# Kernel tuning notes

Hardware: AMD Instinct MI355X
Metric: run time of the kernel (lower is better)

## Reference

```python
import jax, jax.numpy as jnp
import numpy as np

B, HG, WG, D, NH, K = 4, 32, 32, 768, 12, 7
HD = D // NH  # 64


def _neigh_idx(H, W, k):
    # NATTEN semantics: 7x7 window centered at the query, shifted (clamped)
    # at borders so every query has exactly k*k neighbors.
    si = np.clip(np.arange(H) - k // 2, 0, H - k)  # [H] window row starts
    sj = np.clip(np.arange(W) - k // 2, 0, W - k)  # [W] window col starts
    ri = si[:, None] + np.arange(k)[None, :]       # [H, k]
    cj = sj[:, None] + np.arange(k)[None, :]       # [W, k]
    idx = ri[:, None, :, None] * W + cj[None, :, None, :]  # [H, W, k, k]
    return jnp.asarray(idx.reshape(H * W, k * k), dtype=jnp.int32)


def setup_inputs() -> dict:
    key = jax.random.key(0)
    ks = jax.random.split(key, 3)
    s = D ** -0.5
    return {
        "x": jax.random.normal(ks[0], (B, HG * WG, D), dtype=jnp.float32),
        "qkv_w": jax.random.normal(ks[1], (3 * D, D), dtype=jnp.float32) * s,
        "qkv_b": jnp.zeros((3 * D,), dtype=jnp.float32),
        "proj_w": jax.random.normal(ks[2], (D, D), dtype=jnp.float32) * s,
        "proj_b": jnp.zeros((D,), dtype=jnp.float32),
    }


def reference(x, qkv_w, qkv_b, proj_w, proj_b):
    b, n, d = x.shape  # n == HG*WG
    idx = _neigh_idx(HG, WG, K)  # [n, K*K] flat neighbor token indices

    qkv = x @ qkv_w.T + qkv_b                      # [b, n, 3d]
    q, k, v = jnp.split(qkv, 3, axis=-1)
    q = q.reshape(b, n, NH, HD) * (HD ** -0.5)     # [b, n, h, hd]
    k = k.reshape(b, n, NH, HD)
    v = v.reshape(b, n, NH, HD)

    kn = jnp.take(k, idx, axis=1)                  # [b, n, 49, h, hd]
    vn = jnp.take(v, idx, axis=1)                  # [b, n, 49, h, hd]

    scores = jnp.einsum('bnhd,bnkhd->bnhk', q, kn)  # [b, n, h, 49]
    attn = jax.nn.softmax(scores, axis=-1)
    out = jnp.einsum('bnhk,bnkhd->bnhd', attn, vn).reshape(b, n, d)
    return out @ proj_w.T + proj_b
```

## Files before the change

kernel.cpp:

```cpp
#include <hip/hip_runtime.h>


typedef __bf16 bf16x8 __attribute__((ext_vector_type(8)));
typedef short s16x4 __attribute__((ext_vector_type(4)));
typedef float f32x4 __attribute__((ext_vector_type(4)));

__device__ __forceinline__ unsigned short f2bf(float f) {
  unsigned u = __float_as_uint(f);
  u += 0x7fffu + ((u >> 16) & 1u);
  return (unsigned short)(u >> 16);
}

template <typename T>
__device__ __forceinline__ void gld_lds16(const T* g, T* l) {
  __builtin_amdgcn_global_load_lds((const __attribute__((address_space(1))) void*)g,
                                   (__attribute__((address_space(3))) void*)l, 16, 0, 0);
}

__global__ void cvt_kernel(const float* __restrict__ x, const float* __restrict__ w1,
                           const float* __restrict__ w2, unsigned short* __restrict__ xo,
                           unsigned short* __restrict__ w1o, unsigned short* __restrict__ w2o) {
  const int n1 = 4096 * 768 / 4;
  const int n2 = 2304 * 768 / 4;
  const int n3 = 768 * 768 / 4;
  int i = blockIdx.x * 256 + threadIdx.x;
  float4 v;
  unsigned short* dst;
  int o;
  if (i < n1) {
    o = i; v = ((const float4*)x)[o]; dst = xo;
  } else if (i < n1 + n2) {
    o = i - n1; v = ((const float4*)w1)[o]; dst = w1o;
  } else if (i < n1 + n2 + n3) {
    o = i - n1 - n2; v = ((const float4*)w2)[o]; dst = w2o;
  } else {
    return;
  }
  ushort4 r;
  r.x = f2bf(v.x); r.y = f2bf(v.y); r.z = f2bf(v.z); r.w = f2bf(v.w);
  ((ushort4*)dst)[o] = r;
}

template <int MODE>
__global__ __launch_bounds__(256) void gemm_bt(const unsigned short* __restrict__ A,
                                               const unsigned short* __restrict__ Bm,
                                               const float* __restrict__ bias,
                                               unsigned short* __restrict__ obf,
                                               unsigned short* __restrict__ vtout,
                                               float* __restrict__ of32,
                                               int M, int N, int Kd) {
  __shared__ __align__(16) unsigned short sA[2][128 * 32];
  __shared__ __align__(16) unsigned short sB[2][128 * 32];
  const int tid = threadIdx.x;
  const int lane = tid & 63;
  const int wv = tid >> 6;

  constexpr int HX = (MODE == 0) ? 9 : 3;
  constexpr int HY = 8;
  const int lin = blockIdx.y * gridDim.x + blockIdx.x;
  const int xcd = lin & 7, rrr = lin >> 3;
  const int bx = (xcd & 1) * HX + rrr % HX;
  const int by = (xcd >> 1) * HY + rrr / HX;
  const int m0 = by * 128, n0 = bx * 128;

  const int wrow = (wv >> 1) * 64, wcol = (wv & 1) * 64;
  const int lr = lane & 15, lq = lane >> 4;
  const int rchunk = (lq ^ ((lr >> 1) & 3)) * 8;

  f32x4 acc[4][4] = {};

  const int schunk = ((tid & 3) ^ ((tid >> 3) & 3)) * 8;
  const unsigned short* gA = A + (size_t)(m0 + (tid >> 2)) * Kd + schunk;
  const unsigned short* gB = Bm + (size_t)(n0 + (tid >> 2)) * Kd + schunk;

  gld_lds16(gA, &sA[0][tid * 8]);
  gld_lds16(gA + (size_t)64 * Kd, &sA[0][2048 + tid * 8]);
  gld_lds16(gB, &sB[0][tid * 8]);
  gld_lds16(gB + (size_t)64 * Kd, &sB[0][2048 + tid * 8]);
  __syncthreads();

  int cur = 0;
  for (int k0 = 0; k0 < Kd; k0 += 32) {
    const int nxt = k0 + 32;
    if (nxt < Kd) {
      unsigned short* dA = sA[cur ^ 1];
      unsigned short* dB = sB[cur ^ 1];
      gld_lds16(gA + nxt, dA + tid * 8);
      gld_lds16(gA + (size_t)64 * Kd + nxt, dA + 2048 + tid * 8);
      gld_lds16(gB + nxt, dB + tid * 8);
      gld_lds16(gB + (size_t)64 * Kd + nxt, dB + 2048 + tid * 8);
    }
    const unsigned short* cA = sA[cur];
    const unsigned short* cB = sB[cur];
    bf16x8 af[4], bfr[4];
#pragma unroll
    for (int t = 0; t < 4; ++t) {
      af[t] = *(const bf16x8*)(cA + (wrow + t * 16 + lr) * 32 + rchunk);
      bfr[t] = *(const bf16x8*)(cB + (wcol + t * 16 + lr) * 32 + rchunk);
    }
#pragma unroll
    for (int im = 0; im < 4; ++im)
#pragma unroll
      for (int in = 0; in < 4; ++in)
        acc[im][in] = __builtin_amdgcn_mfma_f32_16x16x32_bf16(af[im], bfr[in], acc[im][in], 0, 0, 0);
    __syncthreads();
    cur ^= 1;
  }

  if (MODE == 0) {
    const int sidx = n0 / 768;
    if (sidx == 2) {
#pragma unroll
      for (int im = 0; im < 4; ++im) {
#pragma unroll
        for (int in = 0; in < 4; ++in) {
          int gn = n0 + wcol + in * 16 + lr;
          int rem = gn - 1536;
          int hh = rem >> 6, dd = gn & 63;
          float bsv = bias[gn];
          int gm0 = m0 + wrow + im * 16 + lq * 4;
          ushort4 pk;
          pk.x = f2bf(acc[im][in][0] + bsv);
          pk.y = f2bf(acc[im][in][1] + bsv);
          pk.z = f2bf(acc[im][in][2] + bsv);
          pk.w = f2bf(acc[im][in][3] + bsv);
          *(ushort4*)(vtout + (size_t)(hh * 64 + dd) * 4096 + gm0) = pk;
        }
      }
    } else {
      const float scale = (sidx == 0) ? 0.18033688f : 1.0f;
#pragma unroll
      for (int im = 0; im < 4; ++im) {
#pragma unroll
        for (int in = 0; in < 4; ++in) {
          int gn = n0 + wcol + in * 16 + lr;
          int rem = gn - sidx * 768;
          int hh = rem >> 6, dd = gn & 63;
          float bsv = bias[gn];
#pragma unroll
          for (int r = 0; r < 4; ++r) {
            int gm = m0 + wrow + im * 16 + lq * 4 + r;
            float val = (acc[im][in][r] + bsv) * scale;
            obf[((size_t)(sidx * 12 + hh) * 4096 + gm) * 64 + dd] = f2bf(val);
          }
        }
      }
    }
  } else {
#pragma unroll
    for (int im = 0; im < 4; ++im) {
#pragma unroll
      for (int in = 0; in < 4; ++in) {
        int gn = n0 + wcol + in * 16 + lr;
        float bsv = bias[gn];
#pragma unroll
        for (int r = 0; r < 4; ++r) {
          int gm = m0 + wrow + im * 16 + lq * 4 + r;
          of32[(size_t)gm * N + gn] = acc[im][in][r] + bsv;
        }
      }
    }
  }
}

__global__ __launch_bounds__(256, 2) void natten_kernel(const unsigned short* __restrict__ qkvt,
                                                        unsigned short* __restrict__ aout) {
  __shared__ __align__(16) unsigned short sQ[64 * 64];
  __shared__ __align__(16) unsigned short sK[256 * 64];
  __shared__ __align__(16) unsigned short sVt[64 * 256];
  const int h = blockIdx.x, ip = blockIdx.y, b = blockIdx.z;
  const int i0 = ip * 2;
  const int tid = threadIdx.x, lane = tid & 63, wv = tid >> 6;
  const int lg = lane >> 4, lm = lane & 15;
  int si0 = i0 - 3; si0 = si0 < 0 ? 0 : si0; if (si0 > 25) si0 = 25;
  const int gb = b * 1024;
  const unsigned short* Qg = qkvt + ((size_t)h * 4096 + gb + i0 * 32) * 64;
  const unsigned short* Kg = qkvt + ((size_t)(12 + h) * 4096 + gb) * 64;
  const unsigned short* Vg = qkvt + (size_t)24 * 4096 * 64 + (size_t)h * 64 * 4096 + gb;

#pragma unroll
  for (int it = 0; it < 2; ++it) {
    int f = it * 256 + tid;
    int q = f >> 3, c16 = f & 7;
    uint4 v = *(const uint4*)(Qg + q * 64 + c16 * 8);
    int s = q & 15;
    *(uint2*)(sQ + q * 64 + ((((c16 << 1)) ^ s) << 2)) = make_uint2(v.x, v.y);
    *(uint2*)(sQ + q * 64 + ((((c16 << 1) | 1) ^ s) << 2)) = make_uint2(v.z, v.w);
  }
#pragma unroll
  for (int it = 0; it < 8; ++it) {
    int f = it * 256 + tid;
    int t = f >> 3, c16 = f & 7;
    int wr = t >> 5, c = t & 31;
    int row = si0 + wr; if (row > 31) row = 31;
    uint4 v = *(const uint4*)(Kg + (row * 32 + c) * 64 + c16 * 8);
    int s = t & 15;
    *(uint2*)(sK + t * 64 + ((((c16 << 1)) ^ s) << 2)) = make_uint2(v.x, v.y);
    *(uint2*)(sK + t * 64 + ((((c16 << 1) | 1) ^ s) << 2)) = make_uint2(v.z, v.w);
  }
#pragma unroll
  for (int it = 0; it < 8; ++it) {
    int f = it * 256 + tid;
    int d = f >> 5, tc16 = f & 31;
    int wr = tc16 >> 2;
    int row = si0 + wr; if (row > 31) row = 31;
    uint4 v = *(const uint4*)(Vg + (size_t)d * 4096 + row * 32 + (tc16 & 3) * 8);
    int s = d & 15;
    *(uint2*)(sVt + d * 256 + ((((tc16 << 1)) ^ s) << 2)) = make_uint2(v.x, v.y);
    *(uint2*)(sVt + d * 256 + ((((tc16 << 1) | 1) ^ s) << 2)) = make_uint2(v.z, v.w);
  }
  __syncthreads();

  const int row_sel = wv >> 1;
  const int jhalf = wv & 1;
  const int i = i0 + row_sel;
  int si_w = i - 3; si_w = si_w < 0 ? 0 : si_w; if (si_w > 25) si_w = 25;
  const int toff = (si_w - si0) * 32;
  const int j = jhalf * 16 + lm;
  int sj = j - 3; sj = sj < 0 ? 0 : sj; if (sj > 25) sj = 25;

  float madd[2][4];
#pragma unroll
  for (int p = 0; p < 2; ++p)
#pragma unroll
    for (int r = 0; r < 4; ++r) {
      int c = p * 16 + lg * 4 + r;
      madd[p][r] = (c >= sj && c <= sj + 6) ? 0.f : -1e30f;
    }

  s16x4 qf[4];
  const int qrow = row_sel * 32 + j;
#pragma unroll
  for (int ks = 0; ks < 4; ++ks)
    qf[ks] = *(const s16x4*)(sQ + qrow * 64 + ((((ks << 2) + lg) ^ (qrow & 15)) << 2));

  f32x4 accS[14];
#pragma unroll
  for (int tt = 0; tt < 14; ++tt) {
    f32x4 a = {0.f, 0.f, 0.f, 0.f};
    const int trow = toff + tt * 16 + lm;
    const unsigned short* kr = sK + trow * 64;
    const int sw = trow & 15;
#pragma unroll
    for (int ks = 0; ks < 4; ++ks) {
      s16x4 kf = *(const s16x4*)(kr + ((((ks << 2) + lg) ^ sw) << 2));
      a = __builtin_amdgcn_mfma_f32_16x16x16bf16_1k(kf, qf[ks], a, 0, 0, 0);
    }
    accS[tt] = a;
  }

  float mx = -3e38f;
#pragma unroll
  for (int tt = 0; tt < 14; ++tt)
#pragma unroll
    for (int r = 0; r < 4; ++r) {
      float v = accS[tt][r] + madd[tt & 1][r];
      accS[tt][r] = v;
      mx = fmaxf(mx, v);
    }
  mx = fmaxf(mx, __shfl_xor(mx, 16, 64));
  mx = fmaxf(mx, __shfl_xor(mx, 32, 64));
  float sum = 0.f;
#pragma unroll
  for (int tt = 0; tt < 14; ++tt)
#pragma unroll
    for (int r = 0; r < 4; ++r) {
      float p = exp2f(accS[tt][r] - mx);
      accS[tt][r] = p;
      sum += p;
    }
  sum += __shfl_xor(sum, 16, 64);
  sum += __shfl_xor(sum, 32, 64);
  const float inv = 1.f / sum;

  s16x4 pf[14];
#pragma unroll
  for (int tt = 0; tt < 14; ++tt) {
    union { unsigned u[2]; s16x4 v; } pk;
    pk.u[0] = ((unsigned)f2bf(accS[tt][1]) << 16) | f2bf(accS[tt][0]);
    pk.u[1] = ((unsigned)f2bf(accS[tt][3]) << 16) | f2bf(accS[tt][2]);
    pf[tt] = pk.v;
  }

  f32x4 accO[4] = {};
  const int choff = toff >> 2;
#pragma unroll
  for (int tt = 0; tt < 14; ++tt) {
    const int c8 = choff + tt * 4 + lg;
#pragma unroll
    for (int nt = 0; nt < 4; ++nt) {
      const int d = nt * 16 + lm;
      s16x4 vf = *(const s16x4*)(sVt + d * 256 + ((c8 ^ (d & 15)) << 2));
      accO[nt] = __builtin_amdgcn_mfma_f32_16x16x16bf16_1k(pf[tt], vf, accO[nt], 0, 0, 0);
    }
  }

  float invr[4];
#pragma unroll
  for (int r = 0; r < 4; ++r) invr[r] = __shfl(inv, lg * 4 + r, 64);

  const int tokbase = gb + i * 32 + jhalf * 16;
#pragma unroll
  for (int nt = 0; nt < 4; ++nt)
#pragma unroll
    for (int r = 0; r < 4; ++r) {
      int tok = tokbase + lg * 4 + r;
      aout[(size_t)tok * 768 + h * 64 + nt * 16 + lm] = f2bf(accO[nt][r] * invr[r]);
    }
}

extern "C" void kernel_launch(void* const* d_in, const int* in_sizes, int n_in,
                              void* d_out, int out_size, void* d_ws, size_t ws_size,
                              hipStream_t stream) {
  const float* x      = (const float*)d_in[0];
  const float* qkv_w  = (const float*)d_in[1];
  const float* qkv_b  = (const float*)d_in[2];
  const float* proj_w = (const float*)d_in[3];
  const float* proj_b = (const float*)d_in[4];
  char* ws = (char*)d_ws;

  unsigned short* xb    = (unsigned short*)(ws);
  unsigned short* wqkv  = (unsigned short*)(ws + 6291456);
  unsigned short* wproj = (unsigned short*)(ws + 9830400);
  unsigned short* qkvt  = (unsigned short*)(ws + 11010048);
  unsigned short* attnb = (unsigned short*)(ws + 29884416);
  unsigned short* vt    = qkvt + (size_t)24 * 4096 * 64;
  float* out = (float*)d_out;

  cvt_kernel<<<5376, 256, 0, stream>>>(x, qkv_w, proj_w, xb, wqkv, wproj);
  gemm_bt<0><<<dim3(18, 32), 256, 0, stream>>>(xb, wqkv, qkv_b, qkvt, vt, nullptr, 4096, 2304, 768);
  natten_kernel<<<dim3(12, 16, 4), 256, 0, stream>>>(qkvt, attnb);
  gemm_bt<1><<<dim3(6, 32), 256, 0, stream>>>(attnb, wproj, proj_b, nullptr, nullptr, out, 4096, 768, 768);
}
```

Measured before the change: 145.2 us.

## Share one LDS buffer for K and V in natten, retile projection GEMM

The natten kernel drops the separate Q, K and Vt shared buffers. It loads K and V into registers up front, reads Q straight from global memory, and reuses a single LDS buffer for K and then V with extra barriers between the phases. The smaller LDS footprint allows the launch bound to rise to 3 blocks per CU for higher occupancy and more latency hiding. The output projection GEMM is templated and moved to 64x64 tiles with a larger grid for better CU fill, at the cost of less data reuse per tile and more register pressure in natten.

```diff
diff --git a/kernel.cpp b/kernel.cpp
--- a/kernel.cpp
+++ b/kernel.cpp
@@ -41,7 +41,7 @@
   ((ushort4*)dst)[o] = r;
 }
 
-template <int MODE>
+template <int MODE, int BM, int BN>
 __global__ __launch_bounds__(256) void gemm_bt(const unsigned short* __restrict__ A,
                                                const unsigned short* __restrict__ Bm,
                                                const float* __restrict__ bias,
@@ -49,34 +49,36 @@
                                                unsigned short* __restrict__ vtout,
                                                float* __restrict__ of32,
                                                int M, int N, int Kd) {
-  __shared__ __align__(16) unsigned short sA[2][128 * 32];
-  __shared__ __align__(16) unsigned short sB[2][128 * 32];
+  constexpr int RA = BM / 64, RB = BN / 64;
+  constexpr int MI = BM / 32, NI = BN / 32;
+  __shared__ __align__(16) unsigned short sA[2][BM * 32];
+  __shared__ __align__(16) unsigned short sB[2][BN * 32];
   const int tid = threadIdx.x;
   const int lane = tid & 63;
   const int wv = tid >> 6;
 
-  constexpr int HX = (MODE == 0) ? 9 : 3;
-  constexpr int HY = 8;
+  constexpr int HX = (MODE == 0) ? 9 : 6;
+  constexpr int HY = (MODE == 0) ? 8 : 16;
   const int lin = blockIdx.y * gridDim.x + blockIdx.x;
   const int xcd = lin & 7, rrr = lin >> 3;
   const int bx = (xcd & 1) * HX + rrr % HX;
   const int by = (xcd >> 1) * HY + rrr / HX;
-  const int m0 = by * 128, n0 = bx * 128;
-
-  const int wrow = (wv >> 1) * 64, wcol = (wv & 1) * 64;
+  const int m0 = by * BM, n0 = bx * BN;
+
+  const int wrow = (wv >> 1) * (BM / 2), wcol = (wv & 1) * (BN / 2);
   const int lr = lane & 15, lq = lane >> 4;
   const int rchunk = (lq ^ ((lr >> 1) & 3)) * 8;
 
-  f32x4 acc[4][4] = {};
+  f32x4 acc[MI][NI] = {};
 
   const int schunk = ((tid & 3) ^ ((tid >> 3) & 3)) * 8;
   const unsigned short* gA = A + (size_t)(m0 + (tid >> 2)) * Kd + schunk;
   const unsigned short* gB = Bm + (size_t)(n0 + (tid >> 2)) * Kd + schunk;
 
-  gld_lds16(gA, &sA[0][tid * 8]);
-  gld_lds16(gA + (size_t)64 * Kd, &sA[0][2048 + tid * 8]);
-  gld_lds16(gB, &sB[0][tid * 8]);
-  gld_lds16(gB + (size_t)64 * Kd, &sB[0][2048 + tid * 8]);
+#pragma unroll
+  for (int r = 0; r < RA; ++r) gld_lds16(gA + (size_t)(r * 64) * Kd, &sA[0][r * 2048 + tid * 8]);
+#pragma unroll
+  for (int r = 0; r < RB; ++r) gld_lds16(gB + (size_t)(r * 64) * Kd, &sB[0][r * 2048 + tid * 8]);
   __syncthreads();
 
   int cur = 0;
@@ -85,23 +87,22 @@
     if (nxt < Kd) {
       unsigned short* dA = sA[cur ^ 1];
       unsigned short* dB = sB[cur ^ 1];
-      gld_lds16(gA + nxt, dA + tid * 8);
-      gld_lds16(gA + (size_t)64 * Kd + nxt, dA + 2048 + tid * 8);
-      gld_lds16(gB + nxt, dB + tid * 8);
-      gld_lds16(gB + (size_t)64 * Kd + nxt, dB + 2048 + tid * 8);
+#pragma unroll
+      for (int r = 0; r < RA; ++r) gld_lds16(gA + (size_t)(r * 64) * Kd + nxt, dA + r * 2048 + tid * 8);
+#pragma unroll
+      for (int r = 0; r < RB; ++r) gld_lds16(gB + (size_t)(r * 64) * Kd + nxt, dB + r * 2048 + tid * 8);
     }
     const unsigned short* cA = sA[cur];
     const unsigned short* cB = sB[cur];
-    bf16x8 af[4], bfr[4];
-#pragma unroll
-    for (int t = 0; t < 4; ++t) {
-      af[t] = *(const bf16x8*)(cA + (wrow + t * 16 + lr) * 32 + rchunk);
-      bfr[t] = *(const bf16x8*)(cB + (wcol + t * 16 + lr) * 32 + rchunk);
-    }
-#pragma unroll
-    for (int im = 0; im < 4; ++im)
-#pragma unroll
-      for (int in = 0; in < 4; ++in)
+    bf16x8 af[MI], bfr[NI];
+#pragma unroll
+    for (int t = 0; t < MI; ++t) af[t] = *(const bf16x8*)(cA + (wrow + t * 16 + lr) * 32 + rchunk);
+#pragma unroll
+    for (int t = 0; t < NI; ++t) bfr[t] = *(const bf16x8*)(cB + (wcol + t * 16 + lr) * 32 + rchunk);
+#pragma unroll
+    for (int im = 0; im < MI; ++im)
+#pragma unroll
+      for (int in = 0; in < NI; ++in)
         acc[im][in] = __builtin_amdgcn_mfma_f32_16x16x32_bf16(af[im], bfr[in], acc[im][in], 0, 0, 0);
     __syncthreads();
     cur ^= 1;
@@ -111,9 +112,9 @@
     const int sidx = n0 / 768;
     if (sidx == 2) {
 #pragma unroll
-      for (int im = 0; im < 4; ++im) {
-#pragma unroll
-        for (int in = 0; in < 4; ++in) {
+      for (int im = 0; im < MI; ++im) {
+#pragma unroll
+        for (int in = 0; in < NI; ++in) {
           int gn = n0 + wcol + in * 16 + lr;
           int rem = gn - 1536;
           int hh = rem >> 6, dd = gn & 63;
@@ -130,9 +131,9 @@
     } else {
       const float scale = (sidx == 0) ? 0.18033688f : 1.0f;
 #pragma unroll
-      for (int im = 0; im < 4; ++im) {
-#pragma unroll
-        for (int in = 0; in < 4; ++in) {
+      for (int im = 0; im < MI; ++im) {
+#pragma unroll
+        for (int in = 0; in < NI; ++in) {
           int gn = n0 + wcol + in * 16 + lr;
           int rem = gn - sidx * 768;
           int hh = rem >> 6, dd = gn & 63;
@@ -148,9 +149,9 @@
     }
   } else {
 #pragma unroll
-    for (int im = 0; im < 4; ++im) {
-#pragma unroll
-      for (int in = 0; in < 4; ++in) {
+    for (int im = 0; im < MI; ++im) {
+#pragma unroll
+      for (int in = 0; in < NI; ++in) {
         int gn = n0 + wcol + in * 16 + lr;
         float bsv = bias[gn];
 #pragma unroll
@@ -163,11 +164,9 @@
   }
 }
 
-__global__ __launch_bounds__(256, 2) void natten_kernel(const unsigned short* __restrict__ qkvt,
+__global__ __launch_bounds__(256, 3) void natten_kernel(const unsigned short* __restrict__ qkvt,
                                                         unsigned short* __restrict__ aout) {
-  __shared__ __align__(16) unsigned short sQ[64 * 64];
-  __shared__ __align__(16) unsigned short sK[256 * 64];
-  __shared__ __align__(16) unsigned short sVt[64 * 256];
+  __shared__ __align__(16) unsigned short sKV[256 * 64];
   const int h = blockIdx.x, ip = blockIdx.y, b = blockIdx.z;
   const int i0 = ip * 2;
   const int tid = threadIdx.x, lane = tid & 63, wv = tid >> 6;
@@ -178,38 +177,20 @@
   const unsigned short* Kg = qkvt + ((size_t)(12 + h) * 4096 + gb) * 64;
   const unsigned short* Vg = qkvt + (size_t)24 * 4096 * 64 + (size_t)h * 64 * 4096 + gb;
 
-#pragma unroll
-  for (int it = 0; it < 2; ++it) {
-    int f = it * 256 + tid;
-    int q = f >> 3, c16 = f & 7;
-    uint4 v = *(const uint4*)(Qg + q * 64 + c16 * 8);
-    int s = q & 15;
-    *(uint2*)(sQ + q * 64 + ((((c16 << 1)) ^ s) << 2)) = make_uint2(v.x, v.y);
-    *(uint2*)(sQ + q * 64 + ((((c16 << 1) | 1) ^ s) << 2)) = make_uint2(v.z, v.w);
-  }
+  uint4 kreg[8];
 #pragma unroll
   for (int it = 0; it < 8; ++it) {
-    int f = it * 256 + tid;
-    int t = f >> 3, c16 = f & 7;
-    int wr = t >> 5, c = t & 31;
+    int row = si0 + it; if (row > 31) row = 31;
+    kreg[it] = *(const uint4*)(Kg + (row * 32 + (tid >> 3)) * 64 + (tid & 7) * 8);
+  }
+  uint4 vreg[8];
+#pragma unroll
+  for (int it = 0; it < 8; ++it) {
+    int d = it * 8 + (tid >> 5);
+    int wr = (tid >> 2) & 7;
     int row = si0 + wr; if (row > 31) row = 31;
-    uint4 v = *(const uint4*)(Kg + (row * 32 + c) * 64 + c16 * 8);
-    int s = t & 15;
-    *(uint2*)(sK + t * 64 + ((((c16 << 1)) ^ s) << 2)) = make_uint2(v.x, v.y);
-    *(uint2*)(sK + t * 64 + ((((c16 << 1) | 1) ^ s) << 2)) = make_uint2(v.z, v.w);
-  }
-#pragma unroll
-  for (int it = 0; it < 8; ++it) {
-    int f = it * 256 + tid;
-    int d = f >> 5, tc16 = f & 31;
-    int wr = tc16 >> 2;
-    int row = si0 + wr; if (row > 31) row = 31;
-    uint4 v = *(const uint4*)(Vg + (size_t)d * 4096 + row * 32 + (tc16 & 3) * 8);
-    int s = d & 15;
-    *(uint2*)(sVt + d * 256 + ((((tc16 << 1)) ^ s) << 2)) = make_uint2(v.x, v.y);
-    *(uint2*)(sVt + d * 256 + ((((tc16 << 1) | 1) ^ s) << 2)) = make_uint2(v.z, v.w);
-  }
-  __syncthreads();
+    vreg[it] = *(const uint4*)(Vg + (size_t)d * 4096 + row * 32 + (tid & 3) * 8);
+  }
 
   const int row_sel = wv >> 1;
   const int jhalf = wv & 1;
@@ -219,6 +200,22 @@
   const int j = jhalf * 16 + lm;
   int sj = j - 3; sj = sj < 0 ? 0 : sj; if (sj > 25) sj = 25;
 
+  s16x4 qf[4];
+  const int qrow = row_sel * 32 + j;
+#pragma unroll
+  for (int ks = 0; ks < 4; ++ks)
+    qf[ks] = *(const s16x4*)(Qg + qrow * 64 + ks * 16 + lg * 4);
+
+#pragma unroll
+  for (int it = 0; it < 8; ++it) {
+    int t = it * 32 + (tid >> 3);
+    int c16 = tid & 7;
+    int s = t & 15;
+    *(uint2*)(sKV + t * 64 + ((((c16 << 1)) ^ s) << 2)) = make_uint2(kreg[it].x, kreg[it].y);
+    *(uint2*)(sKV + t * 64 + ((((c16 << 1) | 1) ^ s) << 2)) = make_uint2(kreg[it].z, kreg[it].w);
+  }
+  __syncthreads();
+
   float madd[2][4];
 #pragma unroll
   for (int p = 0; p < 2; ++p)
@@ -228,18 +225,12 @@
       madd[p][r] = (c >= sj && c <= sj + 6) ? 0.f : -1e30f;
     }
 
-  s16x4 qf[4];
-  const int qrow = row_sel * 32 + j;
-#pragma unroll
-  for (int ks = 0; ks < 4; ++ks)
-    qf[ks] = *(const s16x4*)(sQ + qrow * 64 + ((((ks << 2) + lg) ^ (qrow & 15)) << 2));
-
   f32x4 accS[14];
 #pragma unroll
   for (int tt = 0; tt < 14; ++tt) {
     f32x4 a = {0.f, 0.f, 0.f, 0.f};
     const int trow = toff + tt * 16 + lm;
-    const unsigned short* kr = sK + trow * 64;
+    const unsigned short* kr = sKV + trow * 64;
     const int sw = trow & 15;
 #pragma unroll
     for (int ks = 0; ks < 4; ++ks) {
@@ -247,6 +238,16 @@
       a = __builtin_amdgcn_mfma_f32_16x16x16bf16_1k(kf, qf[ks], a, 0, 0, 0);
     }
     accS[tt] = a;
+  }
+  __syncthreads();
+
+#pragma unroll
+  for (int it = 0; it < 8; ++it) {
+    int d = it * 8 + (tid >> 5);
+    int tc16 = tid & 31;
+    int s = d & 15;
+    *(uint2*)(sKV + d * 256 + ((((tc16 << 1)) ^ s) << 2)) = make_uint2(vreg[it].x, vreg[it].y);
+    *(uint2*)(sKV + d * 256 + ((((tc16 << 1) | 1) ^ s) << 2)) = make_uint2(vreg[it].z, vreg[it].w);
   }
 
   float mx = -3e38f;
@@ -281,6 +282,7 @@
     pk.u[1] = ((unsigned)f2bf(accS[tt][3]) << 16) | f2bf(accS[tt][2]);
     pf[tt] = pk.v;
   }
+  __syncthreads();
 
   f32x4 accO[4] = {};
   const int choff = toff >> 2;
@@ -290,7 +292,7 @@
 #pragma unroll
     for (int nt = 0; nt < 4; ++nt) {
       const int d = nt * 16 + lm;
-      s16x4 vf = *(const s16x4*)(sVt + d * 256 + ((c8 ^ (d & 15)) << 2));
+      s16x4 vf = *(const s16x4*)(sKV + d * 256 + ((c8 ^ (d & 15)) << 2));
       accO[nt] = __builtin_amdgcn_mfma_f32_16x16x16bf16_1k(pf[tt], vf, accO[nt], 0, 0, 0);
     }
   }
@@ -328,7 +330,7 @@
   float* out = (float*)d_out;
 
   cvt_kernel<<<5376, 256, 0, stream>>>(x, qkv_w, proj_w, xb, wqkv, wproj);
-  gemm_bt<0><<<dim3(18, 32), 256, 0, stream>>>(xb, wqkv, qkv_b, qkvt, vt, nullptr, 4096, 2304, 768);
+  gemm_bt<0, 128, 128><<<dim3(18, 32), 256, 0, stream>>>(xb, wqkv, qkv_b, qkvt, vt, nullptr, 4096, 2304, 768);
   natten_kernel<<<dim3(12, 16, 4), 256, 0, stream>>>(qkvt, attnb);
-  gemm_bt<1><<<dim3(6, 32), 256, 0, stream>>>(attnb, wproj, proj_b, nullptr, nullptr, out, 4096, 768, 768);
-}
+  gemm_bt<1, 64, 64><<<dim3(12, 64), 256, 0, stream>>>(attnb, wproj, proj_b, nullptr, nullptr, out, 4096, 768, 768);
+}
```

After: 144.1 us. No clear change (-0.8%).
